# Performance work log

Measured on AMD Instinct MI355X. Metric: run time of the kernel, lower is better.

The kernel has to match this reference:

```python
import jax, jax.numpy as jnp
import numpy as np

B, S, H, NH, DH, FF = 8, 512, 768, 12, 64, 3072
EPS = 1e-3  # matches epsilon used in the repo's LayerNormalization


def layer_norm(x, g, b):
    mu = jnp.mean(x, axis=-1, keepdims=True)
    var = jnp.mean(jnp.square(x - mu), axis=-1, keepdims=True)
    return (x - mu) * jax.lax.rsqrt(var + EPS) * g + b


def setup_inputs() -> dict:
    key = jax.random.key(0)
    ks = jax.random.split(key, 12)
    init = lambda k, shp: (jax.random.normal(k, shp, dtype=jnp.float32) * 0.02)
    return {
        "hidden_states": jax.random.normal(ks[0], (B, S, H), dtype=jnp.float32),
        "attention_mask": jnp.ones((B, S), dtype=jnp.int32),
        "Wq": init(ks[1], (H, H)), "bq": jnp.zeros((H,), jnp.float32),
        "Wk": init(ks[2], (H, H)), "bk": jnp.zeros((H,), jnp.float32),
        "Wv": init(ks[3], (H, H)), "bv": jnp.zeros((H,), jnp.float32),
        "Wo": init(ks[4], (H, H)), "bo": jnp.zeros((H,), jnp.float32),
        "ln1_g": jnp.ones((H,), jnp.float32), "ln1_b": jnp.zeros((H,), jnp.float32),
        "W1": init(ks[5], (H, FF)), "b1": jnp.zeros((FF,), jnp.float32),
        "W2": init(ks[6], (FF, H)), "b2": jnp.zeros((H,), jnp.float32),
        "ln2_g": jnp.ones((H,), jnp.float32), "ln2_b": jnp.zeros((H,), jnp.float32),
    }


def reference(hidden_states, attention_mask, Wq, bq, Wk, bk, Wv, bv, Wo, bo,
              ln1_g, ln1_b, W1, b1, W2, b2, ln2_g, ln2_b):
    x = hidden_states  # [B,S,H]
    b, s, h = x.shape
    split = lambda t: t.reshape(b, s, NH, DH).transpose(0, 2, 1, 3)  # [B,NH,S,DH]
    q = split(x @ Wq + bq)
    k = split(x @ Wk + bk)
    v = split(x @ Wv + bv)
    scores = jnp.einsum("bhqd,bhkd->bhqk", q, k) / jnp.sqrt(jnp.float32(DH))
    # BERT-style additive mask: (1 - mask) * -10000, broadcast over heads/queries
    m = attention_mask.astype(jnp.float32)[:, None, None, :]
    scores = scores + (1.0 - m) * -10000.0
    probs = jax.nn.softmax(scores, axis=-1)
    ctx = jnp.einsum("bhqk,bhkd->bhqd", probs, v)
    ctx = ctx.transpose(0, 2, 1, 3).reshape(b, s, h)  # [B,S,H]
    attn_out = ctx @ Wo + bo
    h1 = layer_norm(attn_out + x, ln1_g, ln1_b)
    ff = jax.nn.gelu(h1 @ W1 + b1, approximate=False) @ W2 + b2
    return layer_norm(ff + h1, ln2_g, ln2_b)
```

## Files before the change

### kernel.cpp

```cpp
#include <hip/hip_runtime.h>
#include <hip/hip_bf16.h>

#define H_DIM 768
#define FF_DIM 3072
#define NHEAD 12
#define DHEAD 64
#define SEQ 512
#define TOK 4096

typedef __bf16 bf16;
using bf16x8 = __attribute__((ext_vector_type(8))) __bf16;
using f32x4  = __attribute__((ext_vector_type(4))) float;

static __device__ __forceinline__ f32x4 mfma16(bf16x8 a, bf16x8 b, f32x4 c) {
  return __builtin_amdgcn_mfma_f32_16x16x32_bf16(a, b, c, 0, 0, 0);
}

static __device__ __forceinline__ void gl2lds16(const bf16* g, bf16* l) {
  __builtin_amdgcn_global_load_lds((const __attribute__((address_space(1))) void*)g,
                                   (__attribute__((address_space(3))) void*)l, 16, 0, 0);
}

__global__ __launch_bounds__(256) void cvt_k(const float* __restrict__ in, bf16* __restrict__ out, int n) {
  int i = (blockIdx.x * 256 + threadIdx.x) * 8;
  if (i >= n) return;
  float4 a = *(const float4*)(in + i);
  float4 b = *(const float4*)(in + i + 4);
  bf16x8 o;
  o[0] = (bf16)a.x; o[1] = (bf16)a.y; o[2] = (bf16)a.z; o[3] = (bf16)a.w;
  o[4] = (bf16)b.x; o[5] = (bf16)b.y; o[6] = (bf16)b.z; o[7] = (bf16)b.w;
  *(bf16x8*)(out + i) = o;
}

struct CvtTArgs { const float* in[4]; bf16* out[4]; };
__global__ __launch_bounds__(256) void cvtT_k(CvtTArgs args, int R, int C) {
  __shared__ bf16 tile[32][33];
  const float* in = args.in[blockIdx.z];
  bf16* out = args.out[blockIdx.z];
  int c0 = blockIdx.x * 32, r0 = blockIdx.y * 32;
  int tx = threadIdx.x & 31, ty = threadIdx.x >> 5;
  for (int i = 0; i < 32; i += 8) tile[ty + i][tx] = (bf16)in[(size_t)(r0 + ty + i) * C + c0 + tx];
  __syncthreads();
  for (int i = 0; i < 32; i += 8) out[(size_t)(c0 + ty + i) * R + r0 + tx] = tile[tx][ty + i];
}

struct GemmArgs {
  const bf16* A;
  const bf16* W[3];
  const float* bias[3];
  bf16* outB[3];
  float* outP[2];
  int N, K, nx, ry, kSlices;
};

#define BK 32

template <int MODE>
__global__ __launch_bounds__(256) void gemm_x(GemmArgs args) {
  __shared__ bf16 As[128 * BK];
  __shared__ bf16 Bs[128 * BK];
  int bid = blockIdx.x;
  int xcd = bid & 7, tt = bid >> 3;
  int ry = args.ry;
  int by = xcd * ry + (tt % ry);
  int rest = tt / ry;
  int bx = rest % args.nx;
  int z = rest / args.nx;

  const bf16* A = args.A;
  const bf16* Bt;
  int Kd = args.K, N = args.N;
  int kBeg, kEnd;
  if constexpr (MODE == 2) {
    Bt = args.W[0];
    int ks = Kd / args.kSlices;
    kBeg = z * ks; kEnd = kBeg + ks;
  } else {
    Bt = args.W[z];
    kBeg = 0; kEnd = Kd;
  }
  int m0 = by * 128, n0 = bx * 128;
  int t = threadIdx.x;
  int wid = t >> 6, lane = t & 63, quad = lane >> 4, l16 = lane & 15;
  int wm = wid >> 1, wn = wid & 1;

  f32x4 zero4 = {0.0f, 0.0f, 0.0f, 0.0f};
  f32x4 acc[4][4];
#pragma unroll
  for (int mi = 0; mi < 4; mi++)
#pragma unroll
    for (int ni = 0; ni < 4; ni++) acc[mi][ni] = zero4;

  int ch = wid * 2;
  int rA = lane >> 2;
  int cE = (lane & 3) * 8;
  const bf16* gA0 = A  + (size_t)(m0 + ch * 16 + rA) * Kd + cE;
  const bf16* gA1 = gA0 + (size_t)16 * Kd;
  const bf16* gB0 = Bt + (size_t)(n0 + ch * 16 + rA) * Kd + cE;
  const bf16* gB1 = gB0 + (size_t)16 * Kd;
  bf16* lA0 = As + ch * 512;
  bf16* lA1 = As + ch * 512 + 512;
  bf16* lB0 = Bs + ch * 512;
  bf16* lB1 = Bs + ch * 512 + 512;

  for (int k0 = kBeg; k0 < kEnd; k0 += BK) {
    __syncthreads();
    gl2lds16(gA0 + k0, lA0);
    gl2lds16(gA1 + k0, lA1);
    gl2lds16(gB0 + k0, lB0);
    gl2lds16(gB1 + k0, lB1);
    __syncthreads();
    bf16x8 af[4], bfr[4];
#pragma unroll
    for (int mi = 0; mi < 4; mi++) af[mi] = *(const bf16x8*)&As[(wm * 64 + mi * 16 + l16) * BK + quad * 8];
#pragma unroll
    for (int ni = 0; ni < 4; ni++) bfr[ni] = *(const bf16x8*)&Bs[(wn * 64 + ni * 16 + l16) * BK + quad * 8];
#pragma unroll
    for (int mi = 0; mi < 4; mi++)
#pragma unroll
      for (int ni = 0; ni < 4; ni++) acc[mi][ni] = mfma16(af[mi], bfr[ni], acc[mi][ni]);
  }

  if constexpr (MODE == 2) {
    float* outP = args.outP[z];
#pragma unroll
    for (int mi = 0; mi < 4; mi++) {
#pragma unroll
      for (int r = 0; r < 4; r++) {
        int row = m0 + wm * 64 + mi * 16 + quad * 4 + r;
#pragma unroll
        for (int ni = 0; ni < 4; ni++) {
          int col = n0 + wn * 64 + ni * 16 + l16;
          outP[(size_t)row * N + col] = acc[mi][ni][r];
        }
      }
    }
  } else {
    const float* bias = args.bias[z];
    bf16* outB = args.outB[z];
    float bv[4];
#pragma unroll
    for (int ni = 0; ni < 4; ni++) bv[ni] = bias[n0 + wn * 64 + ni * 16 + l16];
#pragma unroll
    for (int mi = 0; mi < 4; mi++) {
#pragma unroll
      for (int r = 0; r < 4; r++) {
        int row = m0 + wm * 64 + mi * 16 + quad * 4 + r;
#pragma unroll
        for (int ni = 0; ni < 4; ni++) {
          int col = n0 + wn * 64 + ni * 16 + l16;
          float v = acc[mi][ni][r] + bv[ni];
          if constexpr (MODE == 1) v = 0.5f * v * (1.0f + erff(v * 0.70710678118654752f));
          outB[(size_t)row * N + col] = (bf16)v;
        }
      }
    }
  }
}

#define CHK 128
__global__ __launch_bounds__(256) void attn_k(const bf16* __restrict__ Qg, const bf16* __restrict__ Kg,
                                              const bf16* __restrict__ Vg, const int* __restrict__ mask,
                                              bf16* __restrict__ ctx) {
  __shared__ bf16 Ks[CHK][72];
  __shared__ unsigned int Vts[DHEAD][68];
  __shared__ float maskadd[CHK];
  __shared__ bf16 Ps[4][16][136];
  int bh = blockIdx.x;
  int b = bh / NHEAD, h = bh % NHEAD;
  int q0 = blockIdx.y * 64;
  int t = threadIdx.x;
  int wid = t >> 6, lane = t & 63, quad = lane >> 4, l16 = lane & 15;
  size_t base = (size_t)b * SEQ * H_DIM + (size_t)h * DHEAD;

  int qrow = q0 + wid * 16 + l16;
  bf16x8 qf0 = *(const bf16x8*)(Qg + base + (size_t)qrow * H_DIM + quad * 8);
  bf16x8 qf1 = *(const bf16x8*)(Qg + base + (size_t)qrow * H_DIM + 32 + quad * 8);

  f32x4 zero4 = {0.0f, 0.0f, 0.0f, 0.0f};
  f32x4 o[4];
  float m_i[4], l_i[4];
#pragma unroll
  for (int r = 0; r < 4; r++) { o[r] = zero4; m_i[r] = -1e30f; l_i[r] = 0.0f; }

  for (int c0 = 0; c0 < SEQ; c0 += CHK) {
    __syncthreads();
    {
      int row = t >> 1, half = (t & 1) * 32;
      const bf16* g = Kg + base + (size_t)(c0 + row) * H_DIM + half;
      *(bf16x8*)&Ks[row][half]      = *(const bf16x8*)g;
      *(bf16x8*)&Ks[row][half + 8]  = *(const bf16x8*)(g + 8);
      *(bf16x8*)&Ks[row][half + 16] = *(const bf16x8*)(g + 16);
      *(bf16x8*)&Ks[row][half + 24] = *(const bf16x8*)(g + 24);
    }
#pragma unroll
    for (int p = 0; p < 2; ++p) {
      int kp = t & 63;
      int dg = ((t >> 6) + p * 4) * 8;
      const bf16* vp = Vg + base + (size_t)(c0 + 2 * kp) * H_DIM + dg;
      bf16x8 v0 = *(const bf16x8*)vp;
      bf16x8 v1 = *(const bf16x8*)(vp + H_DIM);
      const unsigned short* u0 = (const unsigned short*)&v0;
      const unsigned short* u1 = (const unsigned short*)&v1;
#pragma unroll
      for (int j = 0; j < 8; j++)
        Vts[dg + j][kp] = (unsigned int)u0[j] | ((unsigned int)u1[j] << 16);
    }
    if (t < CHK) maskadd[t] = (1.0f - (float)mask[b * SEQ + c0 + t]) * -10000.0f;
    __syncthreads();

    f32x4 sc[8];
#pragma unroll
    for (int k8 = 0; k8 < 8; k8++) {
      const bf16* krow = &Ks[k8 * 16 + l16][0];
      bf16x8 ka = *(const bf16x8*)(krow + quad * 8);
      bf16x8 kb = *(const bf16x8*)(krow + 32 + quad * 8);
      f32x4 s = mfma16(qf0, ka, zero4);
      sc[k8] = mfma16(qf1, kb, s);
    }
    float madd[8];
#pragma unroll
    for (int k8 = 0; k8 < 8; k8++) madd[k8] = maskadd[k8 * 16 + l16];

#pragma unroll
    for (int r = 0; r < 4; r++) {
      float v[8], mx = -1e30f;
#pragma unroll
      for (int k8 = 0; k8 < 8; k8++) { v[k8] = sc[k8][r] * 0.125f + madd[k8]; mx = fmaxf(mx, v[k8]); }
#pragma unroll
      for (int off = 1; off < 16; off <<= 1) mx = fmaxf(mx, __shfl_xor(mx, off));
      float mnew = fmaxf(m_i[r], mx);
      float alpha = __expf(m_i[r] - mnew);
      m_i[r] = mnew;
      float ps = 0.0f;
#pragma unroll
      for (int k8 = 0; k8 < 8; k8++) { v[k8] = __expf(v[k8] - mnew); ps += v[k8]; }
#pragma unroll
      for (int off = 1; off < 16; off <<= 1) ps += __shfl_xor(ps, off);
      l_i[r] = l_i[r] * alpha + ps;
#pragma unroll
      for (int ni = 0; ni < 4; ni++) o[ni][r] *= alpha;
#pragma unroll
      for (int k8 = 0; k8 < 8; k8++) Ps[wid][quad * 4 + r][k8 * 16 + l16] = (bf16)v[k8];
    }

#pragma unroll
    for (int kt = 0; kt < CHK; kt += 32) {
      bf16x8 pa = *(const bf16x8*)&Ps[wid][l16][kt + quad * 8];
#pragma unroll
      for (int ni = 0; ni < 4; ni++) {
        const bf16* vrow = (const bf16*)&Vts[ni * 16 + l16][0] + kt + quad * 8;
        o[ni] = mfma16(pa, *(const bf16x8*)vrow, o[ni]);
      }
    }
  }
#pragma unroll
  for (int r = 0; r < 4; r++) {
    int row = q0 + wid * 16 + quad * 4 + r;
    float inv = 1.0f / l_i[r];
#pragma unroll
    for (int ni = 0; ni < 4; ni++)
      ctx[base + (size_t)row * H_DIM + ni * 16 + l16] = (bf16)(o[ni][r] * inv);
  }
}

__global__ __launch_bounds__(256) void redln_k(const float* __restrict__ p0, const float* __restrict__ p1,
                                               const float* __restrict__ resF, const bf16* __restrict__ resB,
                                               const float* __restrict__ bias,
                                               const float* __restrict__ g, const float* __restrict__ bta,
                                               bf16* __restrict__ outB, float* __restrict__ outF) {
  int row = blockIdx.x, t = threadIdx.x;
  size_t base = (size_t)row * H_DIM;
  float v[3], s = 0.0f, sq = 0.0f;
#pragma unroll
  for (int i = 0; i < 3; i++) {
    int c = t + i * 256;
    float r = resF ? resF[base + c] : (float)resB[base + c];
    float x = p0[base + c] + p1[base + c] + bias[c] + r;
    v[i] = x; s += x; sq += x * x;
  }
#pragma unroll
  for (int off = 32; off >= 1; off >>= 1) { s += __shfl_down(s, off); sq += __shfl_down(sq, off); }
  __shared__ float ssum[4], ssq[4], smu, srs;
  int lane = t & 63, w = t >> 6;
  if (lane == 0) { ssum[w] = s; ssq[w] = sq; }
  __syncthreads();
  if (t == 0) {
    float S = ssum[0] + ssum[1] + ssum[2] + ssum[3];
    float Q = ssq[0] + ssq[1] + ssq[2] + ssq[3];
    float mu = S * (1.0f / H_DIM);
    float var = Q * (1.0f / H_DIM) - mu * mu;
    smu = mu;
    srs = rsqrtf(var + 1e-3f);
  }
  __syncthreads();
  float mu = smu, rs = srs;
#pragma unroll
  for (int i = 0; i < 3; i++) {
    int c = t + i * 256;
    float y = (v[i] - mu) * rs * g[c] + bta[c];
    if (outB) outB[base + c] = (bf16)y;
    if (outF) outF[base + c] = y;
  }
}

extern "C" void kernel_launch(void* const* d_in, const int* in_sizes, int n_in,
                              void* d_out, int out_size, void* d_ws, size_t ws_size,
                              hipStream_t stream) {
  const float* x    = (const float*)d_in[0];
  const int*   mask = (const int*)d_in[1];
  const float* Wq = (const float*)d_in[2];  const float* bq = (const float*)d_in[3];
  const float* Wk = (const float*)d_in[4];  const float* bk = (const float*)d_in[5];
  const float* Wv = (const float*)d_in[6];  const float* bv = (const float*)d_in[7];
  const float* Wo = (const float*)d_in[8];  const float* bo = (const float*)d_in[9];
  const float* ln1g = (const float*)d_in[10]; const float* ln1b = (const float*)d_in[11];
  const float* W1 = (const float*)d_in[12]; const float* b1 = (const float*)d_in[13];
  const float* W2 = (const float*)d_in[14]; const float* b2 = (const float*)d_in[15];
  const float* ln2g = (const float*)d_in[16]; const float* ln2b = (const float*)d_in[17];
  float* out = (float*)d_out;
  (void)ws_size; (void)in_sizes; (void)n_in; (void)out_size;

  char* w = (char*)d_ws;
  const size_t SZ_TH  = 6291456;
  const size_t SZ_THF = 12582912;
  const size_t SZ_W   = 1179648;
  bf16* xB   = (bf16*)(w);
  bf16* QB   = (bf16*)(w + SZ_TH);
  bf16* KB   = (bf16*)(w + 2 * SZ_TH);
  bf16* VB   = (bf16*)(w + 3 * SZ_TH);
  float* P1s0 = (float*)(w);
  float* P1s1 = (float*)(w + SZ_THF);
  bf16* FFA  = (bf16*)(w);
  bf16* CTX  = (bf16*)(w + 4 * SZ_TH);
  bf16* H1   = CTX;
  bf16* WqT  = (bf16*)(w + 5 * SZ_TH);
  bf16* WkT  = (bf16*)(w + 5 * SZ_TH + SZ_W);
  bf16* WvT  = (bf16*)(w + 5 * SZ_TH + 2 * SZ_W);
  bf16* WoT  = (bf16*)(w + 5 * SZ_TH + 3 * SZ_W);
  bf16* W1T  = (bf16*)(w + 5 * SZ_TH + 4 * SZ_W);
  float* P2s0 = (float*)(w + 5 * SZ_TH);
  float* P2s1 = (float*)(w + 5 * SZ_TH + SZ_THF);
  bf16* W2T  = (bf16*)(w + 5 * SZ_TH + 2 * SZ_THF);

  dim3 tb(256);

  cvt_k<<<(TOK * H_DIM) / 2048, tb, 0, stream>>>(x, xB, TOK * H_DIM);
  CvtTArgs ct = {};
  ct.in[0] = Wq; ct.in[1] = Wk; ct.in[2] = Wv; ct.in[3] = Wo;
  ct.out[0] = WqT; ct.out[1] = WkT; ct.out[2] = WvT; ct.out[3] = WoT;
  cvtT_k<<<dim3(24, 24, 4), tb, 0, stream>>>(ct, H_DIM, H_DIM);
  CvtTArgs c1 = {}; c1.in[0] = W1; c1.out[0] = W1T;
  cvtT_k<<<dim3(96, 24, 1), tb, 0, stream>>>(c1, H_DIM, FF_DIM);
  CvtTArgs c2 = {}; c2.in[0] = W2; c2.out[0] = W2T;
  cvtT_k<<<dim3(24, 96, 1), tb, 0, stream>>>(c2, FF_DIM, H_DIM);

  GemmArgs ga = {};
  ga.A = xB; ga.N = H_DIM; ga.K = H_DIM; ga.nx = 6; ga.ry = 4; ga.kSlices = 1;
  ga.W[0] = WqT; ga.W[1] = WkT; ga.W[2] = WvT;
  ga.bias[0] = bq; ga.bias[1] = bk; ga.bias[2] = bv;
  ga.outB[0] = QB; ga.outB[1] = KB; ga.outB[2] = VB;
  gemm_x<0><<<576, tb, 0, stream>>>(ga);

  attn_k<<<dim3(8 * NHEAD, SEQ / 64), tb, 0, stream>>>(QB, KB, VB, mask, CTX);

  GemmArgs go = {};
  go.A = CTX; go.N = H_DIM; go.K = H_DIM; go.nx = 6; go.ry = 4; go.kSlices = 2;
  go.W[0] = WoT; go.outP[0] = P1s0; go.outP[1] = P1s1;
  gemm_x<2><<<384, tb, 0, stream>>>(go);

  redln_k<<<TOK, tb, 0, stream>>>(P1s0, P1s1, x, nullptr, bo, ln1g, ln1b, H1, nullptr);

  GemmArgs g1 = {};
  g1.A = H1; g1.N = FF_DIM; g1.K = H_DIM; g1.nx = 24; g1.ry = 4; g1.kSlices = 1;
  g1.W[0] = W1T; g1.bias[0] = b1; g1.outB[0] = FFA;
  gemm_x<1><<<768, tb, 0, stream>>>(g1);

  GemmArgs g2 = {};
  g2.A = FFA; g2.N = H_DIM; g2.K = FF_DIM; g2.nx = 6; g2.ry = 4; g2.kSlices = 2;
  g2.W[0] = W2T; g2.outP[0] = P2s0; g2.outP[1] = P2s1;
  gemm_x<2><<<384, tb, 0, stream>>>(g2);

  redln_k<<<TOK, tb, 0, stream>>>(P2s0, P2s1, nullptr, H1, b2, ln2g, ln2b, nullptr, out);
}
```

Baseline: 286.0 us.

## Shrink GEMM tile to 128x64 and double the K step to 64

Changes the GEMM block tile from 128x128 to 128x64 and loads two 32-wide K slabs per iteration. This halves the number of barrier pairs per K and doubles the grid size for better occupancy and CU coverage on the small GEMMs. In exchange, each block gets less reuse of A, so global traffic for A rises, and per-wave MFMA work per LDS read shrinks.

```diff
diff --git a/kernel.cpp b/kernel.cpp
--- a/kernel.cpp
+++ b/kernel.cpp
@@ -53,12 +53,10 @@
   int N, K, nx, ry, kSlices;
 };
 
-#define BK 32
-
 template <int MODE>
 __global__ __launch_bounds__(256) void gemm_x(GemmArgs args) {
-  __shared__ bf16 As[128 * BK];
-  __shared__ bf16 Bs[128 * BK];
+  __shared__ bf16 As[2][128 * 32];
+  __shared__ bf16 Bs[2][64 * 32];
   int bid = blockIdx.x;
   int xcd = bid & 7, tt = bid >> 3;
   int ry = args.ry;
@@ -79,46 +77,51 @@
     Bt = args.W[z];
     kBeg = 0; kEnd = Kd;
   }
-  int m0 = by * 128, n0 = bx * 128;
+  int m0 = by * 128, n0 = bx * 64;
   int t = threadIdx.x;
   int wid = t >> 6, lane = t & 63, quad = lane >> 4, l16 = lane & 15;
   int wm = wid >> 1, wn = wid & 1;
 
   f32x4 zero4 = {0.0f, 0.0f, 0.0f, 0.0f};
-  f32x4 acc[4][4];
+  f32x4 acc[4][2];
 #pragma unroll
   for (int mi = 0; mi < 4; mi++)
 #pragma unroll
-    for (int ni = 0; ni < 4; ni++) acc[mi][ni] = zero4;
-
-  int ch = wid * 2;
+    for (int ni = 0; ni < 2; ni++) acc[mi][ni] = zero4;
+
   int rA = lane >> 2;
   int cE = (lane & 3) * 8;
-  const bf16* gA0 = A  + (size_t)(m0 + ch * 16 + rA) * Kd + cE;
+  const bf16* gA0 = A  + (size_t)(m0 + wid * 32 + rA) * Kd + cE;
   const bf16* gA1 = gA0 + (size_t)16 * Kd;
-  const bf16* gB0 = Bt + (size_t)(n0 + ch * 16 + rA) * Kd + cE;
-  const bf16* gB1 = gB0 + (size_t)16 * Kd;
-  bf16* lA0 = As + ch * 512;
-  bf16* lA1 = As + ch * 512 + 512;
-  bf16* lB0 = Bs + ch * 512;
-  bf16* lB1 = Bs + ch * 512 + 512;
-
-  for (int k0 = kBeg; k0 < kEnd; k0 += BK) {
+  const bf16* gB0 = Bt + (size_t)(n0 + wid * 16 + rA) * Kd + cE;
+  bf16* lA0 = &As[0][wid * 1024];
+  bf16* lA1 = &As[0][wid * 1024 + 512];
+  bf16* lB0 = &Bs[0][wid * 512];
+  bf16* lA2 = &As[1][wid * 1024];
+  bf16* lA3 = &As[1][wid * 1024 + 512];
+  bf16* lB1 = &Bs[1][wid * 512];
+
+  for (int k0 = kBeg; k0 < kEnd; k0 += 64) {
     __syncthreads();
     gl2lds16(gA0 + k0, lA0);
     gl2lds16(gA1 + k0, lA1);
     gl2lds16(gB0 + k0, lB0);
-    gl2lds16(gB1 + k0, lB1);
+    gl2lds16(gA0 + k0 + 32, lA2);
+    gl2lds16(gA1 + k0 + 32, lA3);
+    gl2lds16(gB0 + k0 + 32, lB1);
     __syncthreads();
-    bf16x8 af[4], bfr[4];
-#pragma unroll
-    for (int mi = 0; mi < 4; mi++) af[mi] = *(const bf16x8*)&As[(wm * 64 + mi * 16 + l16) * BK + quad * 8];
-#pragma unroll
-    for (int ni = 0; ni < 4; ni++) bfr[ni] = *(const bf16x8*)&Bs[(wn * 64 + ni * 16 + l16) * BK + quad * 8];
-#pragma unroll
-    for (int mi = 0; mi < 4; mi++)
-#pragma unroll
-      for (int ni = 0; ni < 4; ni++) acc[mi][ni] = mfma16(af[mi], bfr[ni], acc[mi][ni]);
+#pragma unroll
+    for (int h = 0; h < 2; h++) {
+      bf16x8 af[4], bfr[2];
+#pragma unroll
+      for (int mi = 0; mi < 4; mi++) af[mi] = *(const bf16x8*)&As[h][(wm * 64 + mi * 16 + l16) * 32 + quad * 8];
+#pragma unroll
+      for (int ni = 0; ni < 2; ni++) bfr[ni] = *(const bf16x8*)&Bs[h][(wn * 32 + ni * 16 + l16) * 32 + quad * 8];
+#pragma unroll
+      for (int mi = 0; mi < 4; mi++)
+#pragma unroll
+        for (int ni = 0; ni < 2; ni++) acc[mi][ni] = mfma16(af[mi], bfr[ni], acc[mi][ni]);
+    }
   }
 
   if constexpr (MODE == 2) {
@@ -129,8 +132,8 @@
       for (int r = 0; r < 4; r++) {
         int row = m0 + wm * 64 + mi * 16 + quad * 4 + r;
 #pragma unroll
-        for (int ni = 0; ni < 4; ni++) {
-          int col = n0 + wn * 64 + ni * 16 + l16;
+        for (int ni = 0; ni < 2; ni++) {
+          int col = n0 + wn * 32 + ni * 16 + l16;
           outP[(size_t)row * N + col] = acc[mi][ni][r];
         }
       }
@@ -138,17 +141,17 @@
   } else {
     const float* bias = args.bias[z];
     bf16* outB = args.outB[z];
-    float bv[4];
-#pragma unroll
-    for (int ni = 0; ni < 4; ni++) bv[ni] = bias[n0 + wn * 64 + ni * 16 + l16];
+    float bv[2];
+#pragma unroll
+    for (int ni = 0; ni < 2; ni++) bv[ni] = bias[n0 + wn * 32 + ni * 16 + l16];
 #pragma unroll
     for (int mi = 0; mi < 4; mi++) {
 #pragma unroll
       for (int r = 0; r < 4; r++) {
         int row = m0 + wm * 64 + mi * 16 + quad * 4 + r;
 #pragma unroll
-        for (int ni = 0; ni < 4; ni++) {
-          int col = n0 + wn * 64 + ni * 16 + l16;
+        for (int ni = 0; ni < 2; ni++) {
+          int col = n0 + wn * 32 + ni * 16 + l16;
           float v = acc[mi][ni][r] + bv[ni];
           if constexpr (MODE == 1) v = 0.5f * v * (1.0f + erff(v * 0.70710678118654752f));
           outB[(size_t)row * N + col] = (bf16)v;
@@ -355,30 +358,30 @@
   cvtT_k<<<dim3(24, 96, 1), tb, 0, stream>>>(c2, FF_DIM, H_DIM);
 
   GemmArgs ga = {};
-  ga.A = xB; ga.N = H_DIM; ga.K = H_DIM; ga.nx = 6; ga.ry = 4; ga.kSlices = 1;
+  ga.A = xB; ga.N = H_DIM; ga.K = H_DIM; ga.nx = 12; ga.ry = 4; ga.kSlices = 1;
   ga.W[0] = WqT; ga.W[1] = WkT; ga.W[2] = WvT;
   ga.bias[0] = bq; ga.bias[1] = bk; ga.bias[2] = bv;
   ga.outB[0] = QB; ga.outB[1] = KB; ga.outB[2] = VB;
-  gemm_x<0><<<576, tb, 0, stream>>>(ga);
+  gemm_x<0><<<1152, tb, 0, stream>>>(ga);
 
   attn_k<<<dim3(8 * NHEAD, SEQ / 64), tb, 0, stream>>>(QB, KB, VB, mask, CTX);
 
   GemmArgs go = {};
-  go.A = CTX; go.N = H_DIM; go.K = H_DIM; go.nx = 6; go.ry = 4; go.kSlices = 2;
+  go.A = CTX; go.N = H_DIM; go.K = H_DIM; go.nx = 12; go.ry = 4; go.kSlices = 2;
   go.W[0] = WoT; go.outP[0] = P1s0; go.outP[1] = P1s1;
-  gemm_x<2><<<384, tb, 0, stream>>>(go);
+  gemm_x<2><<<768, tb, 0, stream>>>(go);
 
   redln_k<<<TOK, tb, 0, stream>>>(P1s0, P1s1, x, nullptr, bo, ln1g, ln1b, H1, nullptr);
 
   GemmArgs g1 = {};
-  g1.A = H1; g1.N = FF_DIM; g1.K = H_DIM; g1.nx = 24; g1.ry = 4; g1.kSlices = 1;
+  g1.A = H1; g1.N = FF_DIM; g1.K = H_DIM; g1.nx = 48; g1.ry = 4; g1.kSlices = 1;
   g1.W[0] = W1T; g1.bias[0] = b1; g1.outB[0] = FFA;
-  gemm_x<1><<<768, tb, 0, stream>>>(g1);
+  gemm_x<1><<<1536, tb, 0, stream>>>(g1);
 
   GemmArgs g2 = {};
-  g2.A = FFA; g2.N = H_DIM; g2.K = FF_DIM; g2.nx = 6; g2.ry = 4; g2.kSlices = 2;
+  g2.A = FFA; g2.N = H_DIM; g2.K = FF_DIM; g2.nx = 12; g2.ry = 4; g2.kSlices = 2;
   g2.W[0] = W2T; g2.outP[0] = P2s0; g2.outP[1] = P2s1;
-  gemm_x<2><<<384, tb, 0, stream>>>(g2);
+  gemm_x<2><<<768, tb, 0, stream>>>(g2);
 
   redln_k<<<TOK, tb, 0, stream>>>(P2s0, P2s1, nullptr, H1, b2, ln2g, ln2b, nullptr, out);
 }
```

Measured after the change: 277.5 us. 1.03x faster.
